# Kernel tuning notes

Hardware: AMD Instinct MI355X
Metric: run time of the kernel (lower is better)

The kernel has to match this reference:

```python
import jax, jax.numpy as jnp
import numpy as np


@jax.custom_vjp
def binary_act(x):
    # sign forward, straight-through (clipped) backward, matching BinaryActivation
    return jnp.sign(x)

def _ba_fwd(x):
    return jnp.sign(x), x

def _ba_bwd(x, g):
    return (jnp.where((x >= -1.0) & (x <= 1.0), g, 0.0),)

binary_act.defvjp(_ba_fwd, _ba_bwd)


def conv2d(x, w, b, pad, groups):
    # x: NCHW, w: OIHW
    y = jax.lax.conv_general_dilated(
        x, w, window_strides=(1, 1), padding=[(pad, pad), (pad, pad)],
        feature_group_count=groups,
        dimension_numbers=("NCHW", "OIHW", "NCHW"))
    return y + b[None, :, None, None]


def bconv(x, w, b, pad, groups):
    # Binary_conv2d: weights and bias binarized via sign (no STE on weights in torch either)
    return conv2d(x, jnp.sign(w), jnp.sign(b), pad, groups)


def maxpool2(x):
    return jax.lax.reduce_window(x, -jnp.inf, jax.lax.max,
                                 (1, 1, 2, 2), (1, 1, 2, 2), "VALID")


def setup_inputs() -> dict:
    key = jax.random.key(0)
    ks = jax.random.split(key, 14)
    d = {}
    d["x"] = jax.random.normal(ks[0], (1024, 3, 32, 32), dtype=jnp.float32)
    # conv1: depthwise 3x3 (groups=3) then 1x1 3->128
    d["w1_dw"] = jax.random.normal(ks[1], (3, 1, 3, 3), dtype=jnp.float32) * 0.1
    d["b1_dw"] = jax.random.normal(ks[2], (3,), dtype=jnp.float32) * 0.1
    d["w1_pw"] = jax.random.normal(ks[3], (128, 3, 1, 1), dtype=jnp.float32) * 0.1
    d["b1_pw"] = jax.random.normal(ks[4], (128,), dtype=jnp.float32) * 0.1
    # conv2: depthwise 3x3 (groups=128) then 1x1 128->256
    d["w2_dw"] = jax.random.normal(ks[5], (128, 1, 3, 3), dtype=jnp.float32) * 0.1
    d["b2_dw"] = jax.random.normal(ks[6], (128,), dtype=jnp.float32) * 0.1
    d["w2_pw"] = jax.random.normal(ks[7], (256, 128, 1, 1), dtype=jnp.float32) * 0.1
    d["b2_pw"] = jax.random.normal(ks[8], (256,), dtype=jnp.float32) * 0.1
    # fc layers (full precision weights, sign applied to fc1 output only)
    d["fc1_w"] = jax.random.normal(ks[9], (1024, 256 * 8 * 8), dtype=jnp.float32) * (1.0 / np.sqrt(256 * 8 * 8))
    d["fc1_b"] = jnp.zeros((1024,), dtype=jnp.float32)
    d["fc2_w"] = jax.random.normal(ks[10], (10, 1024), dtype=jnp.float32) * (1.0 / np.sqrt(1024.0))
    d["fc2_b"] = jnp.zeros((10,), dtype=jnp.float32)
    return d


def reference(x, w1_dw, b1_dw, w1_pw, b1_pw, w2_dw, b2_dw, w2_pw, b2_pw,
              fc1_w, fc1_b, fc2_w, fc2_b):
    h = bconv(x, w1_dw, b1_dw, pad=1, groups=3)        # [B,3,32,32]
    h = bconv(h, w1_pw, b1_pw, pad=0, groups=1)        # [B,128,32,32]
    h = maxpool2(binary_act(h))                        # [B,128,16,16]
    h = bconv(h, w2_dw, b2_dw, pad=1, groups=128)      # [B,128,16,16]
    h = bconv(h, w2_pw, b2_pw, pad=0, groups=1)        # [B,256,16,16]
    h = maxpool2(binary_act(h))                        # [B,256,8,8]
    h = h.reshape(h.shape[0], -1)                      # [B,16384]
    h = binary_act(h @ fc1_w.T + fc1_b)                # [B,1024]
    return h @ fc2_w.T + fc2_b                         # [B,10]
```

## Files before the change

kernel.cpp:

```cpp
#include <hip/hip_runtime.h>


__device__ __forceinline__ int fsign(float v)  { return (v > 0.f) - (v < 0.f); }
__device__ __forceinline__ int dsign(double v) { return (v > 0.0) - (v < 0.0); }

typedef int v4i __attribute__((ext_vector_type(4)));

__device__ __forceinline__ void async16(const signed char* g, signed char* l) {
    __builtin_amdgcn_global_load_lds(
        (const __attribute__((address_space(1))) void*)g,
        (__attribute__((address_space(3))) void*)l, 16, 0, 0);
}

__global__ void kprep2(const float* __restrict__ w2pw, const float* __restrict__ b2pw,
                       signed char* __restrict__ w2s, int* __restrict__ b2adj)
{
    int o = blockIdx.x * 64 + threadIdx.x;
    int rs = 0;
    for (int cq = 0; cq < 32; cq++) {
        float4 w = *(const float4*)(w2pw + (size_t)o * 128 + cq * 4);
        int s0 = fsign(w.x), s1 = fsign(w.y), s2 = fsign(w.z), s3 = fsign(w.w);
        rs += s0 + s1 + s2 + s3;
        int pk = (s0 & 0xff) | ((s1 & 0xff) << 8) | ((s2 & 0xff) << 16) | ((s3 & 0xff) << 24);
        *(int*)(w2s + (size_t)o * 128 + cq * 4) = pk;
    }
    b2adj[o] = fsign(b2pw[o]) - 32 * rs;
}

__global__ __launch_bounds__(256, 4) void k13_fused(
    const float* __restrict__ x,
    const float* __restrict__ w1dw, const float* __restrict__ b1dw,
    const float* __restrict__ w1pw, const float* __restrict__ b1pw,
    const float* __restrict__ w2dw, const float* __restrict__ b2dw,
    const signed char* __restrict__ w2s, const int* __restrict__ b2adj,
    signed char* __restrict__ hT2)
{
    __shared__ __align__(16) signed char Ps[32768];
    __shared__ __align__(16) signed char Uni[5120];
    __shared__ int sb2adj[256];
    __shared__ float sdw[27], sbdw[3];
    __shared__ unsigned char spidx[128];

    signed char* sw4  = Uni;
    signed char* sdb2 = Uni + 1152;
    signed char* Os   = Uni;

    int t = threadIdx.x, l = t & 63, wid = t >> 6;
    int n = blockIdx.x;

    if (t < 27) sdw[t] = (float)fsign(w1dw[t]);
    if (t < 3)  sbdw[t] = (float)fsign(b1dw[t]);
    if (t < 128) {
        int b0 = w1pw[t * 3 + 0] > 0.f;
        int b1 = w1pw[t * 3 + 1] > 0.f;
        int b2 = w1pw[t * 3 + 2] > 0.f;
        int b3 = b1pw[t] > 0.f;
        spidx[t] = (unsigned char)(b0 | (b1 << 1) | (b2 << 2) | (b3 << 3));
    }
    for (int i = t; i < 1152; i += 256) {
        int c = i & 127, tap = i >> 7;
        sw4[tap * 128 + c] = (signed char)fsign(w2dw[c * 9 + tap]);
    }
    if (t < 128) sdb2[t] = (signed char)(fsign(b2dw[t]) + 1);
    sb2adj[t] = b2adj[t];
    __syncthreads();

    {
        int px = t & 15, py = t >> 4;
        double h[3][4];
        const float* xb = x + (size_t)n * 3 * 1024;
        #pragma unroll
        for (int c = 0; c < 3; c++) {
            const float* xc = xb + c * 1024;
            #pragma unroll
            for (int dy = 0; dy < 2; dy++)
            #pragma unroll
            for (int dx = 0; dx < 2; dx++) {
                int y = 2 * py + dy, xx = 2 * px + dx;
                double acc = (double)sbdw[c];
                #pragma unroll
                for (int ky = 0; ky < 3; ky++) {
                    int yy = y + ky - 1;
                    if (yy < 0 || yy > 31) continue;
                    #pragma unroll
                    for (int kx = 0; kx < 3; kx++) {
                        int xxx = xx + kx - 1;
                        if (xxx < 0 || xxx > 31) continue;
                        acc += (double)sdw[c * 9 + ky * 3 + kx] * (double)xc[yy * 32 + xxx];
                    }
                }
                h[c][dy * 2 + dx] = acc;
            }
        }

        double tv[4][4];
        #pragma unroll
        for (int q = 0; q < 4; q++) {
            double u = h[0][q] + h[1][q];
            double v = h[0][q] - h[1][q];
            tv[0][q] = v - h[2][q];
            tv[1][q] = u - h[2][q];
            tv[2][q] = v + h[2][q];
            tv[3][q] = u + h[2][q];
        }
        int mpack = 0;
        #pragma unroll
        for (int bp = 0; bp < 4; bp++) {
            int mxP = -2, mnP = 2, mxM = -2, mnM = 2;
            #pragma unroll
            for (int q = 0; q < 4; q++) {
                int sP = dsign(tv[bp][q] + 1.0);
                int sM = dsign(tv[bp][q] - 1.0);
                mxP = max(mxP, sP); mnP = min(mnP, sP);
                mxM = max(mxM, sM); mnM = min(mnM, sM);
            }
            int pat1 = 1 | (bp << 1);
            int pat0 = (~pat1) & 7;
            mpack |= (mxP + 1)   << (2 * (pat1 | 8));
            mpack |= (mxM + 1)   << (2 * pat1);
            mpack |= ((-mnM) + 1) << (2 * (pat0 | 8));
            mpack |= ((-mnP) + 1) << (2 * pat0);
        }

        signed char* prow = Ps + t * 128;
        const int* pint = (const int*)spidx;
        for (int ob = 0; ob < 32; ob++) {
            int pw = pint[ob];
            int cur = 0;
            #pragma unroll
            for (int e = 0; e < 4; e++) {
                int pi = (pw >> (8 * e)) & 15;
                int mv = ((mpack >> (pi * 2)) & 3) - 1;
                cur |= (mv & 0xff) << (8 * e);
            }
            int ad = (((ob >> 2) ^ (t & 7)) << 4) + (ob & 3) * 4;
            *(int*)(prow + ad) = cur;
        }
    }
    __syncthreads();

    int frow = l & 15;

    v4i af[4][2];
    #pragma unroll
    for (int ks = 0; ks < 2; ks++) {
        int c0 = ks * 64 + (l >> 4) * 16;
        int cc = c0 >> 4;
        int4 w4[9];
        #pragma unroll
        for (int tap = 0; tap < 9; tap++)
            w4[tap] = *(const int4*)&sw4[tap * 128 + c0];
        int4 sdbv = *(const int4*)&sdb2[c0];

        #pragma unroll
        for (int i = 0; i < 4; i++) {
            int r = (wid * 4 + i) * 16 + frow;
            int py = r >> 5, px2 = (r >> 2) & 7, dy = (r >> 1) & 1, dx = r & 1;
            int y = 2 * py + dy, xq = 2 * px2 + dx;
            int4 cnt = (int4){0, 0, 0, 0};
            #pragma unroll
            for (int ky = 0; ky < 3; ky++) {
                int yy = y + ky - 1;
                int yc = min(max(yy, 0), 15);
                #pragma unroll
                for (int kx = 0; kx < 3; kx++) {
                    int xx2 = xq + kx - 1;
                    int xc = min(max(xx2, 0), 15);
                    int inb = ((yy == yc) && (xx2 == xc)) ? 0x01010101 : 0;
                    int p = yc * 16 + xc;
                    int4 v = *(const int4*)&Ps[p * 128 + ((cc ^ (p & 7)) * 16)];
                    int4 w = w4[ky * 3 + kx];
                    cnt.x += ((v.x ^ w.x) >> 1) & inb;
                    cnt.y += ((v.y ^ w.y) >> 1) & inb;
                    cnt.z += ((v.z ^ w.z) >> 1) & inb;
                    cnt.w += ((v.w ^ w.w) >> 1) & inb;
                }
            }
            int valid = (1 + (y > 0) + (y < 15)) * (1 + (xq > 0) + (xq < 15));
            int mb = (valid + 31) * 0x01010101;
            int4 u;
            u.x = sdbv.x + mb - (cnt.x + cnt.x);
            u.y = sdbv.y + mb - (cnt.y + cnt.y);
            u.z = sdbv.z + mb - (cnt.z + cnt.z);
            u.w = sdbv.w + mb - (cnt.w + cnt.w);
            af[i][ks] = (v4i){u.x, u.y, u.z, u.w};
        }
    }

    for (int oc = 0; oc < 4; oc++) {
        v4i acc[4][4];
        #pragma unroll
        for (int i = 0; i < 4; i++)
            #pragma unroll
            for (int jt = 0; jt < 4; jt++) acc[i][jt] = (v4i){0, 0, 0, 0};

        #pragma unroll
        for (int ks = 0; ks < 2; ks++) {
            v4i bf[4];
            #pragma unroll
            for (int jt = 0; jt < 4; jt++)
                bf[jt] = *(const v4i*)(w2s + (size_t)(oc * 64 + jt * 16 + frow) * 128
                                       + ks * 64 + (l >> 4) * 16);
            __builtin_amdgcn_s_setprio(1);
            #pragma unroll
            for (int i = 0; i < 4; i++)
                #pragma unroll
                for (int jt = 0; jt < 4; jt++)
                    acc[i][jt] = __builtin_amdgcn_mfma_i32_16x16x64_i8(af[i][ks], bf[jt], acc[i][jt], 0, 0, 0);
            __builtin_amdgcn_s_setprio(0);
        }

        __syncthreads();
        #pragma unroll
        for (int jt = 0; jt < 4; jt++) {
            int o_l = jt * 16 + frow;
            int bia = sb2adj[oc * 64 + o_l];
            #pragma unroll
            for (int i = 0; i < 4; i++) {
                int mx = -2;
                #pragma unroll
                for (int rr = 0; rr < 4; rr++) {
                    int p = acc[i][jt][rr] + bia;
                    int s = (p > 0) - (p < 0);
                    mx = s > mx ? s : mx;
                }
                int pp = (wid * 4 + i) * 4 + (l >> 4);
                Os[o_l * 80 + pp] = (signed char)mx;
            }
        }
        __syncthreads();
        *(int4*)&hT2[(size_t)n * 16384 + oc * 4096 + t * 16]
            = *(const int4*)&Os[(t >> 2) * 80 + (t & 3) * 16];
    }
}

__global__ void kprep(const float* __restrict__ fc1w, signed char* __restrict__ BL)
{
    int t = threadIdx.x;
    int b = blockIdx.x;
    int j = b >> 4, kb = b & 15;
    int k0 = kb * 1024 + t * 4;
    float4 w = *(const float4*)(fc1w + (size_t)j * 16384 + k0);
    float we[4] = {w.x, w.y, w.z, w.w};
    int out[4] = {0, 0, 0, 0};
    #pragma unroll
    for (int e = 0; e < 4; e++) {
        int q = (int)rint((double)we[e] * 4294967296.0);
        q = min(max(q, -266338304), 266338304);
        int d0 = ((q + 64) & 127) - 64; q = (q - d0) >> 7;
        int d1 = ((q + 64) & 127) - 64; q = (q - d1) >> 7;
        int d2 = ((q + 64) & 127) - 64; q = (q - d2) >> 7;
        int d3 = q;
        out[0] |= (d0 & 0xff) << (8 * e);
        out[1] |= (d1 & 0xff) << (8 * e);
        out[2] |= (d2 & 0xff) << (8 * e);
        out[3] |= (d3 & 0xff) << (8 * e);
    }
    #pragma unroll
    for (int m = 0; m < 4; m++)
        *(int*)(BL + (size_t)(j * 4 + m) * 16384 + k0) = out[m];
}

__global__ __launch_bounds__(512, 2) void k4a_fc1(
    const signed char* __restrict__ hT2, const signed char* __restrict__ BL,
    double* __restrict__ Pd)
{
    __shared__ __align__(16) signed char smem[98304];
    int t = threadIdx.x, l = t & 63, wid = t >> 6;
    int nb0 = blockIdx.y * 128, jb0 = blockIdx.x * 256;
    int kh = blockIdx.z, k0 = kh * 8192;
    int ksw = wid >> 2;
    int wn0 = ((wid >> 1) & 1) * 64, wj0 = (wid & 1) * 128;

    int srow = l >> 3;
    int sseg = ((l & 7) ^ srow) * 16;
    const signed char* gA = hT2 + (size_t)(nb0 + wid * 16 + srow) * 16384 + k0 + sseg;
    const signed char* gB = BL  + (size_t)(jb0 + wid * 32 + srow) * 16384 + k0 + sseg;

    v4i acc[4][8];
    #pragma unroll
    for (int i = 0; i < 4; i++)
        #pragma unroll
        for (int q = 0; q < 8; q++) acc[i][q] = (v4i){0, 0, 0, 0};

    {
        signed char* As = smem;
        signed char* Bs = smem + 16384;
        #pragma unroll
        for (int c = 0; c < 2; c++)
            async16(gA + (size_t)c * 8 * 16384, As + (wid * 16 + c * 8) * 128);
        #pragma unroll
        for (int c = 0; c < 4; c++)
            async16(gB + (size_t)c * 8 * 16384, Bs + (wid * 32 + c * 8) * 128);
    }

    int sw = (((ksw * 4) + (l >> 4)) ^ (l & 7)) * 16;

    for (int it = 0; it < 64; it++) {
        __syncthreads();
        if (it + 1 < 64) {
            int kt = (it + 1) * 128;
            signed char* As = smem + ((it + 1) & 1) * 49152;
            signed char* Bs = As + 16384;
            #pragma unroll
            for (int c = 0; c < 2; c++)
                async16(gA + (size_t)c * 8 * 16384 + kt, As + (wid * 16 + c * 8) * 128);
            #pragma unroll
            for (int c = 0; c < 4; c++)
                async16(gB + (size_t)c * 8 * 16384 + kt, Bs + (wid * 32 + c * 8) * 128);
        }
        const signed char* As = smem + (it & 1) * 49152;
        const signed char* Bs = As + 16384;
        v4i af[4], bf[8];
        #pragma unroll
        for (int i = 0; i < 4; i++)
            af[i] = *(const v4i*)&As[(wn0 + i * 16 + (l & 15)) * 128 + sw];
        #pragma unroll
        for (int q = 0; q < 8; q++)
            bf[q] = *(const v4i*)&Bs[(wj0 + q * 16 + (l & 15)) * 128 + sw];
        #pragma unroll
        for (int i = 0; i < 4; i++)
            #pragma unroll
            for (int q = 0; q < 8; q++)
                acc[i][q] = __builtin_amdgcn_mfma_i32_16x16x64_i8(af[i], bf[q], acc[i][q], 0, 0, 0);
    }

    __syncthreads();
    int* S = (int*)smem;
    #pragma unroll
    for (int h = 0; h < 2; h++) {
        if (h) __syncthreads();
        if (ksw == 0 && wn0 == h * 64) {
            #pragma unroll
            for (int i = 0; i < 4; i++)
                #pragma unroll
                for (int q = 0; q < 8; q++)
                    #pragma unroll
                    for (int rr = 0; rr < 4; rr++)
                        S[(i * 16 + (l >> 4) * 4 + rr) * 256 + (wj0 + q * 16 + (l & 15))]
                            = acc[i][q][rr];
        }
        __syncthreads();
        if (ksw == 1 && wn0 == h * 64) {
            #pragma unroll
            for (int i = 0; i < 4; i++)
                #pragma unroll
                for (int q = 0; q < 8; q++)
                    #pragma unroll
                    for (int rr = 0; rr < 4; rr++)
                        S[(i * 16 + (l >> 4) * 4 + rr) * 256 + (wj0 + q * 16 + (l & 15))]
                            += acc[i][q][rr];
        }
        __syncthreads();
        #pragma unroll
        for (int e = 0; e < 8; e++) {
            int idx = t * 8 + e;
            int n_l = idx >> 6, j_l = idx & 63;
            int4 s = *(const int4*)&S[n_l * 256 + j_l * 4];
            double val = (double)s.x + 128.0 * (double)s.y
                       + 16384.0 * (double)s.z + 2097152.0 * (double)s.w;
            Pd[(size_t)kh * 1048576 + (size_t)(nb0 + h * 64 + n_l) * 1024
               + blockIdx.x * 64 + j_l] = val;
        }
    }
}

__global__ __launch_bounds__(256) void k45_comb_fc2(
    const double* __restrict__ Pd, const float* __restrict__ fc1b,
    const float* __restrict__ fc2w, const float* __restrict__ fc2b,
    float* __restrict__ out)
{
    __shared__ double sj[1024];
    __shared__ double pw[4][10];
    int t = threadIdx.x, n = blockIdx.x;
    const double SCALE = 1.0 / 4294967296.0;

    #pragma unroll
    for (int rep = 0; rep < 4; rep++) {
        int j = rep * 256 + t;
        double v = Pd[(size_t)n * 1024 + j] + Pd[1048576 + (size_t)n * 1024 + j];
        double p = v * SCALE + (double)fc1b[j];
        sj[j] = (double)((p > 0.0) - (p < 0.0));
    }
    __syncthreads();

    int j0 = t * 4;
    double s0 = sj[j0], s1 = sj[j0 + 1], s2 = sj[j0 + 2], s3 = sj[j0 + 3];
    double acc[10];
    #pragma unroll
    for (int m = 0; m < 10; m++) {
        float4 w = *(const float4*)(fc2w + (size_t)m * 1024 + j0);
        acc[m] = s0 * (double)w.x + s1 * (double)w.y + s2 * (double)w.z + s3 * (double)w.w;
    }
    #pragma unroll
    for (int off = 32; off > 0; off >>= 1)
        #pragma unroll
        for (int m = 0; m < 10; m++)
            acc[m] += __shfl_down(acc[m], off);
    if ((t & 63) == 0)
        #pragma unroll
        for (int m = 0; m < 10; m++) pw[t >> 6][m] = acc[m];
    __syncthreads();
    if (t < 10)
        out[n * 10 + t] = (float)(pw[0][t] + pw[1][t] + pw[2][t] + pw[3][t] + (double)fc2b[t]);
}

__global__ __launch_bounds__(512) void k4_fc1_mfma(
    const signed char* __restrict__ hT2, const signed char* __restrict__ BL,
    const float* __restrict__ fc1b, signed char* __restrict__ hs)
{
    __shared__ __align__(16) signed char smem[65536];
    int t = threadIdx.x, l = t & 63, wid = t >> 6;
    int nb0 = blockIdx.y * 128, jb0 = blockIdx.x * 128;
    int wn0 = (wid >> 1) * 32;
    int wj0 = (wid & 1) * 64;

    int srow = l >> 3;
    int sseg = ((l & 7) ^ srow) * 16;
    const signed char* gA = hT2 + (size_t)(nb0 + wid * 16 + srow) * 16384 + sseg;
    const signed char* gB = BL  + (size_t)(jb0 + wid * 16 + srow) * 16384 + sseg;

    v4i acc[2][4];
    #pragma unroll
    for (int i = 0; i < 2; i++)
        #pragma unroll
        for (int q = 0; q < 4; q++) acc[i][q] = (v4i){0, 0, 0, 0};

    {
        signed char* As = smem;
        signed char* Bs = smem + 16384;
        #pragma unroll
        for (int i = 0; i < 2; i++) {
            async16(gA + (size_t)i * 8 * 16384, As + (wid * 16 + i * 8) * 128);
            async16(gB + (size_t)i * 8 * 16384, Bs + (wid * 16 + i * 8) * 128);
        }
    }

    for (int it = 0; it < 128; it++) {
        __syncthreads();
        if (it + 1 < 128) {
            int kt = (it + 1) * 128;
            signed char* As = smem + ((it + 1) & 1) * 32768;
            signed char* Bs = As + 16384;
            #pragma unroll
            for (int i = 0; i < 2; i++) {
                async16(gA + (size_t)i * 8 * 16384 + kt, As + (wid * 16 + i * 8) * 128);
                async16(gB + (size_t)i * 8 * 16384 + kt, Bs + (wid * 16 + i * 8) * 128);
            }
        }
        const signed char* As = smem + (it & 1) * 32768;
        const signed char* Bs = As + 16384;
        #pragma unroll
        for (int ks = 0; ks < 2; ks++) {
            int sw = (((ks * 4) + (l >> 4)) ^ (l & 7)) * 16;
            v4i af[2], bf[4];
            #pragma unroll
            for (int i = 0; i < 2; i++)
                af[i] = *(const v4i*)&As[(wn0 + i * 16 + (l & 15)) * 128 + sw];
            #pragma unroll
            for (int q = 0; q < 4; q++)
                bf[q] = *(const v4i*)&Bs[(wj0 + q * 16 + (l & 15)) * 128 + sw];
            #pragma unroll
            for (int i = 0; i < 2; i++)
                #pragma unroll
                for (int q = 0; q < 4; q++)
                    acc[i][q] = __builtin_amdgcn_mfma_i32_16x16x64_i8(af[i], bf[q], acc[i][q], 0, 0, 0);
        }
    }

    __syncthreads();
    int* S = (int*)smem;
    #pragma unroll
    for (int i = 0; i < 2; i++)
        #pragma unroll
        for (int q = 0; q < 4; q++)
            #pragma unroll
            for (int rr = 0; rr < 4; rr++) {
                int n_l  = wn0 + i * 16 + (l >> 4) * 4 + rr;
                int jm_l = wj0 + q * 16 + (l & 15);
                S[n_l * 128 + jm_l] = acc[i][q][rr];
            }
    __syncthreads();

    const double SCALE = 1.0 / 4294967296.0;
    #pragma unroll
    for (int i = 0; i < 8; i++) {
        int idx = t * 8 + i;
        int n_l = idx >> 5, j_l = idx & 31;
        int4 s = *(const int4*)&S[n_l * 128 + j_l * 4];
        double val = (double)s.x + 128.0 * (double)s.y
                   + 16384.0 * (double)s.z + 2097152.0 * (double)s.w;
        int j = blockIdx.x * 32 + j_l;
        double p = val * SCALE + (double)fc1b[j];
        hs[(size_t)(nb0 + n_l) * 1024 + j] = (signed char)((p > 0.0) - (p < 0.0));
    }
}

__global__ void k5_fc2(const signed char* __restrict__ hs,
                       const float* __restrict__ fc2w, const float* __restrict__ fc2b,
                       float* __restrict__ out)
{
    int idx = blockIdx.x * 64 + threadIdx.x;
    if (idx >= 10240) return;
    int n = idx / 10, m = idx - n * 10;
    const signed char* hr = hs + (size_t)n * 1024;
    const float* wr = fc2w + (size_t)m * 1024;
    double acc = (double)fc2b[m];
    for (int jb = 0; jb < 1024; jb += 16) {
        int4 hv = *(const int4*)(hr + jb);
        int wd[4] = {hv.x, hv.y, hv.z, hv.w};
        #pragma unroll
        for (int u = 0; u < 4; u++)
            #pragma unroll
            for (int e = 0; e < 4; e++)
                acc += (double)(signed char)(wd[u] >> (8 * e)) * (double)wr[jb + u * 4 + e];
    }
    out[idx] = (float)acc;
}

extern "C" void kernel_launch(void* const* d_in, const int* in_sizes, int n_in,
                              void* d_out, int out_size, void* d_ws, size_t ws_size,
                              hipStream_t stream)
{
    const float* x    = (const float*)d_in[0];
    const float* w1dw = (const float*)d_in[1];
    const float* b1dw = (const float*)d_in[2];
    const float* w1pw = (const float*)d_in[3];
    const float* b1pw = (const float*)d_in[4];
    const float* w2dw = (const float*)d_in[5];
    const float* b2dw = (const float*)d_in[6];
    const float* w2pw = (const float*)d_in[7];
    const float* b2pw = (const float*)d_in[8];
    const float* fc1w = (const float*)d_in[9];
    const float* fc1b = (const float*)d_in[10];
    const float* fc2w = (const float*)d_in[11];
    const float* fc2b = (const float*)d_in[12];
    float* out = (float*)d_out;

    char* ws = (char*)d_ws;
    signed char* hT2      = (signed char*)(ws + 67108864);
    signed char* w2s      = (signed char*)(ws + 83886080);
    int*         b2adj    = (int*)(ws + 83886080 + 32768);
    signed char* BL       = (signed char*)(ws);
    signed char* hs       = (signed char*)(ws + 83886080 + 1048576);
    double*      Pd       = (double*)(ws + 84934656);
    bool split = ws_size >= (size_t)84934656 + 16777216;

    hipLaunchKernelGGL(kprep2,    dim3(4),     dim3(64),  0, stream,
                       w2pw, b2pw, w2s, b2adj);
    hipLaunchKernelGGL(k13_fused, dim3(1024),  dim3(256), 0, stream,
                       x, w1dw, b1dw, w1pw, b1pw, w2dw, b2dw, w2s, b2adj, hT2);
    hipLaunchKernelGGL(kprep,     dim3(16384), dim3(256), 0, stream,
                       fc1w, BL);
    if (split) {
        hipLaunchKernelGGL(k4a_fc1,      dim3(16, 8, 2), dim3(512), 0, stream,
                           hT2, BL, Pd);
        hipLaunchKernelGGL(k45_comb_fc2, dim3(1024),     dim3(256), 0, stream,
                           Pd, fc1b, fc2w, fc2b, out);
    } else {
        hipLaunchKernelGGL(k4_fc1_mfma, dim3(32, 8), dim3(512), 0, stream,
                           hT2, BL, fc1b, hs);
        hipLaunchKernelGGL(k5_fc2,      dim3(160),   dim3(64),  0, stream,
                           hs, fc2w, fc2b, out);
    }
}
```

Before: 324.6 us.

## Merge fc1 weight quantization blocks into fused conv kernel grid

The fc1 weight-quantization kernel is folded into the conv kernel's grid: of every 17 blocks, one runs the conv pipeline for one image and sixteen quantize fc1 weights, so the memory-bound prep overlaps with the compute-bound conv work and one launch is dropped. The conv output staging now writes all four output chunks into separate regions of the reused Ps buffer, with a single barrier before the stores instead of two barriers per chunk. This adds a small branch per block and, because the shared buffer is larger, quantization blocks reserve the conv kernel's full shared memory footprint, which could limit how many fit per CU.

```diff
diff --git a/kernel.cpp b/kernel.cpp
--- a/kernel.cpp
+++ b/kernel.cpp
@@ -27,26 +27,54 @@
     b2adj[o] = fsign(b2pw[o]) - 32 * rs;
 }
 
-__global__ __launch_bounds__(256, 4) void k13_fused(
+__global__ __launch_bounds__(256, 4) void k13p_fused(
     const float* __restrict__ x,
     const float* __restrict__ w1dw, const float* __restrict__ b1dw,
     const float* __restrict__ w1pw, const float* __restrict__ b1pw,
     const float* __restrict__ w2dw, const float* __restrict__ b2dw,
     const signed char* __restrict__ w2s, const int* __restrict__ b2adj,
-    signed char* __restrict__ hT2)
+    signed char* __restrict__ hT2,
+    const float* __restrict__ fc1w, signed char* __restrict__ BL)
 {
     __shared__ __align__(16) signed char Ps[32768];
-    __shared__ __align__(16) signed char Uni[5120];
+    __shared__ __align__(16) signed char sw4[1152];
+    __shared__ signed char sdb2[128];
     __shared__ int sb2adj[256];
     __shared__ float sdw[27], sbdw[3];
     __shared__ unsigned char spidx[128];
 
-    signed char* sw4  = Uni;
-    signed char* sdb2 = Uni + 1152;
-    signed char* Os   = Uni;
-
-    int t = threadIdx.x, l = t & 63, wid = t >> 6;
-    int n = blockIdx.x;
+    int t = threadIdx.x;
+    int bid = blockIdx.x;
+    int q17 = bid / 17;
+
+    if (bid - q17 * 17 != 0) {
+        int b = bid - q17 - 1;
+        int j = b >> 4, kb = b & 15;
+        int k0 = kb * 1024 + t * 4;
+        float4 w = *(const float4*)(fc1w + (size_t)j * 16384 + k0);
+        float we[4] = {w.x, w.y, w.z, w.w};
+        int out[4] = {0, 0, 0, 0};
+        #pragma unroll
+        for (int e = 0; e < 4; e++) {
+            int q = (int)rint((double)we[e] * 4294967296.0);
+            q = min(max(q, -266338304), 266338304);
+            int d0 = ((q + 64) & 127) - 64; q = (q - d0) >> 7;
+            int d1 = ((q + 64) & 127) - 64; q = (q - d1) >> 7;
+            int d2 = ((q + 64) & 127) - 64; q = (q - d2) >> 7;
+            int d3 = q;
+            out[0] |= (d0 & 0xff) << (8 * e);
+            out[1] |= (d1 & 0xff) << (8 * e);
+            out[2] |= (d2 & 0xff) << (8 * e);
+            out[3] |= (d3 & 0xff) << (8 * e);
+        }
+        #pragma unroll
+        for (int m = 0; m < 4; m++)
+            *(int*)(BL + (size_t)(j * 4 + m) * 16384 + k0) = out[m];
+        return;
+    }
+
+    int l = t & 63, wid = t >> 6;
+    int n = q17;
 
     if (t < 27) sdw[t] = (float)fsign(w1dw[t]);
     if (t < 3)  sbdw[t] = (float)fsign(b1dw[t]);
@@ -186,6 +214,7 @@
             af[i][ks] = (v4i){u.x, u.y, u.z, u.w};
         }
     }
+    __syncthreads();
 
     for (int oc = 0; oc < 4; oc++) {
         v4i acc[4][4];
@@ -210,7 +239,7 @@
             __builtin_amdgcn_s_setprio(0);
         }
 
-        __syncthreads();
+        signed char* Osp = Ps + oc * 5120;
         #pragma unroll
         for (int jt = 0; jt < 4; jt++) {
             int o_l = jt * 16 + frow;
@@ -225,40 +254,16 @@
                     mx = s > mx ? s : mx;
                 }
                 int pp = (wid * 4 + i) * 4 + (l >> 4);
-                Os[o_l * 80 + pp] = (signed char)mx;
-            }
-        }
-        __syncthreads();
+                Osp[o_l * 80 + pp] = (signed char)mx;
+            }
+        }
+    }
+    __syncthreads();
+
+    #pragma unroll
+    for (int oc = 0; oc < 4; oc++)
         *(int4*)&hT2[(size_t)n * 16384 + oc * 4096 + t * 16]
-            = *(const int4*)&Os[(t >> 2) * 80 + (t & 3) * 16];
-    }
-}
-
-__global__ void kprep(const float* __restrict__ fc1w, signed char* __restrict__ BL)
-{
-    int t = threadIdx.x;
-    int b = blockIdx.x;
-    int j = b >> 4, kb = b & 15;
-    int k0 = kb * 1024 + t * 4;
-    float4 w = *(const float4*)(fc1w + (size_t)j * 16384 + k0);
-    float we[4] = {w.x, w.y, w.z, w.w};
-    int out[4] = {0, 0, 0, 0};
-    #pragma unroll
-    for (int e = 0; e < 4; e++) {
-        int q = (int)rint((double)we[e] * 4294967296.0);
-        q = min(max(q, -266338304), 266338304);
-        int d0 = ((q + 64) & 127) - 64; q = (q - d0) >> 7;
-        int d1 = ((q + 64) & 127) - 64; q = (q - d1) >> 7;
-        int d2 = ((q + 64) & 127) - 64; q = (q - d2) >> 7;
-        int d3 = q;
-        out[0] |= (d0 & 0xff) << (8 * e);
-        out[1] |= (d1 & 0xff) << (8 * e);
-        out[2] |= (d2 & 0xff) << (8 * e);
-        out[3] |= (d3 & 0xff) << (8 * e);
-    }
-    #pragma unroll
-    for (int m = 0; m < 4; m++)
-        *(int*)(BL + (size_t)(j * 4 + m) * 16384 + k0) = out[m];
+            = *(const int4*)&Ps[oc * 5120 + (t >> 2) * 80 + (t & 3) * 16];
 }
 
 __global__ __launch_bounds__(512, 2) void k4a_fc1(
@@ -546,11 +551,10 @@
     double*      Pd       = (double*)(ws + 84934656);
     bool split = ws_size >= (size_t)84934656 + 16777216;
 
-    hipLaunchKernelGGL(kprep2,    dim3(4),     dim3(64),  0, stream,
+    hipLaunchKernelGGL(kprep2,     dim3(4),     dim3(64),  0, stream,
                        w2pw, b2pw, w2s, b2adj);
-    hipLaunchKernelGGL(k13_fused, dim3(1024),  dim3(256), 0, stream,
-                       x, w1dw, b1dw, w1pw, b1pw, w2dw, b2dw, w2s, b2adj, hT2);
-    hipLaunchKernelGGL(kprep,     dim3(16384), dim3(256), 0, stream,
+    hipLaunchKernelGGL(k13p_fused, dim3(17408), dim3(256), 0, stream,
+                       x, w1dw, b1dw, w1pw, b1pw, w2dw, b2dw, w2s, b2adj, hT2,
                        fc1w, BL);
     if (split) {
         hipLaunchKernelGGL(k4a_fc1,      dim3(16, 8, 2), dim3(512), 0, stream,
```

After: 357.0 us. +10.0%, slower.
